# Optimization experiments

Measured on AMD Instinct MI355X. Metric: run time of the kernel, lower is better.

The kernel has to match this reference:

```python
import jax, jax.numpy as jnp
import numpy as np

B, OBS, ACT, NT, E = 4096, 512, 64, 10, 16
DREP, DH, DK = 1024, 1024, 512  # rep dim, expert hidden, key/value dim


def setup_inputs() -> dict:
    key = jax.random.key(0)
    ks = jax.random.split(key, 24)
    s = 0.02
    state_core = jax.random.normal(ks[0], (B, OBS), jnp.float32)
    task_ids = jax.random.randint(ks[1], (B,), 0, NT)
    onehot = jax.nn.one_hot(task_ids, NT, dtype=jnp.float32)
    state = jnp.concatenate([state_core, onehot], axis=-1)  # [B, OBS+NT]
    act = jax.random.normal(ks[2], (B, ACT), jnp.float32)
    return {
        "state": state,
        "act": act,
        "rep_W0": s * jax.random.normal(ks[3], (OBS + ACT, DREP), jnp.float32),
        "rep_b0": jnp.zeros((DREP,), jnp.float32),
        "rep_W1": s * jax.random.normal(ks[4], (DREP, DREP), jnp.float32),
        "rep_b1": jnp.zeros((DREP,), jnp.float32),
        "emb": 0.5 * jnp.ones((NT, DK), jnp.float32),
        "Wk0": s * jax.random.normal(ks[5], (E, DREP, DH), jnp.float32),
        "bk0": jnp.zeros((E, DH), jnp.float32),
        "Wk1": s * jax.random.normal(ks[6], (E, DH, DK), jnp.float32),
        "bk1": jnp.zeros((E, DK), jnp.float32),
        "Wv0": s * jax.random.normal(ks[7], (E, DREP, DH), jnp.float32),
        "bv0": jnp.zeros((E, DH), jnp.float32),
        "Wv1": s * jax.random.normal(ks[8], (E, DH, DK), jnp.float32),
        "bv1": jnp.zeros((E, DK), jnp.float32),
        "Wt0": s * jax.random.normal(ks[9], (DK, 512), jnp.float32),
        "bt0": jnp.zeros((512,), jnp.float32),
        "Wt1": s * jax.random.normal(ks[10], (512, 256), jnp.float32),
        "bt1": jnp.zeros((256,), jnp.float32),
        "Wt2": s * jax.random.normal(ks[11], (256, 1), jnp.float32),
        "bt2": jnp.zeros((1,), jnp.float32),
    }


def reference(state, act, rep_W0, rep_b0, rep_W1, rep_b1, emb,
              Wk0, bk0, Wk1, bk1, Wv0, bv0, Wv1, bv1,
              Wt0, bt0, Wt1, bt1, Wt2, bt2):
    num_tasks = emb.shape[0]
    task = jnp.argmax(state[:, -num_tasks:], axis=-1)  # one-hot -> index (== torch.nonzero)
    s = state[:, :-num_tasks]
    # representation: mlp([obs+act, 1024, 1024]) -> relu then identity
    x = jnp.concatenate([s, act], axis=-1)
    rep = jax.nn.relu(x @ rep_W0 + rep_b0) @ rep_W1 + rep_b1  # [B, DREP]
    query = jnp.tanh(emb[task])  # [B, DK]
    # all experts batched (original loops in Python over E tiny MLPs)
    hk = jax.nn.relu(jnp.einsum('bd,edh->ebh', rep, Wk0) + bk0[:, None, :])
    keys = jnp.einsum('ebh,ehk->ebk', hk, Wk1) + bk1[:, None, :]   # [E,B,DK]
    hv = jax.nn.relu(jnp.einsum('bd,edh->ebh', rep, Wv0) + bv0[:, None, :])
    vals = jnp.einsum('ebh,ehk->ebk', hv, Wv1) + bv1[:, None, :]   # [E,B,DK]
    logits = jnp.einsum('bk,ebk->be', query, keys)                 # [B,E]
    attn = jax.nn.softmax(logits, axis=1)
    tower_in = jnp.einsum('be,ebk->bk', attn, vals)                # [B,DK]
    h = jax.nn.relu(tower_in @ Wt0 + bt0)
    h = jax.nn.relu(h @ Wt1 + bt1)
    q = jnp.squeeze(h @ Wt2 + bt2, -1)                             # [B]
    expert_loss = -jnp.mean(
        jnp.sum(jnp.clip(jnp.log(attn + 1e-10), -6.0, 0.0), axis=-1) * 0.3)
    return q, expert_loss
```

## Files before the change

kernel.cpp:

```cpp
#include <hip/hip_runtime.h>
#include <cstdint>
#include <cstddef>

#define NB   4096
#define OBS  512
#define NACT 64
#define NT   10
#define NE   16
#define DREP 1024
#define DH   1024
#define DK   512
#define SLD  (OBS + NT)
#define XK   (OBS + NACT)

typedef short s8v __attribute__((ext_vector_type(8)));
typedef float f4v __attribute__((ext_vector_type(4)));

__device__ __forceinline__ unsigned short f2bf(float f) {
  union { float f; unsigned int u; } v; v.f = f;
  unsigned int u = v.u;
  unsigned int r = (u + 0x7FFFu + ((u >> 16) & 1u)) >> 16;
  return (unsigned short)r;
}
__device__ __forceinline__ float bf2f(unsigned short h) {
  union { unsigned int u; float f; } v; v.u = ((unsigned int)h) << 16;
  return v.f;
}

__device__ __forceinline__ void gload_lds16(const unsigned short* gp, const unsigned short* lp) {
  __builtin_amdgcn_global_load_lds(
      (const __attribute__((address_space(1))) void*)(uintptr_t)gp,
      (__attribute__((address_space(3))) void*)(unsigned int)(uintptr_t)lp,
      16, 0, 0);
}

template <int BM, int BN, int MODE, int RELU, int LDA, int LDB, int KK>
__global__ void __launch_bounds__(256)
gemm_k(const unsigned short* __restrict__ A,
       const unsigned short* __restrict__ Bt,
       const float* __restrict__ bias,
       unsigned short* __restrict__ outB, int ldo,
       const float* __restrict__ qk1, const int* __restrict__ task,
       float* __restrict__ logits, int eBase,
       const float* __restrict__ attn, float* __restrict__ cio)
{
  constexpr int FM = BM / 32;
  constexpr int FN = BN / 32;
  constexpr int CA = BM / 64;
  constexpr int CB = BN / 64;

  __shared__ __align__(16) unsigned short As[BM * 32];
  __shared__ __align__(16) unsigned short Bs[BN * 32];

  const int tid  = threadIdx.x;
  const int wave = tid >> 6;
  const int lane = tid & 63;
  const int wm = wave >> 1, wn = wave & 1;

  const int rowBase = blockIdx.x * BM;
  const int colBase = blockIdx.y * BN;

  int eg = 0;
  if (MODE == 1) {
    eg = blockIdx.z;
    Bt  += (size_t)eg * (DREP * DH);
    bias += eg * DH;
    qk1 += (size_t)eg * (NT * DH);
  }
  if (MODE == 2) {
    eg = eBase + blockIdx.z;
    Bt  += (size_t)eg * (DREP * DH);
    bias += eg * DH;
    outB += (size_t)blockIdx.z * DH;
  }
  if (MODE == 3) {
    int kz = blockIdx.z;
    A  += (size_t)kz * KK;
    Bt += (size_t)kz * KK;
  }

  f4v acc[FM][FN];
#pragma unroll
  for (int m = 0; m < FM; ++m)
#pragma unroll
    for (int n = 0; n < FN; ++n) acc[m][n] = f4v{0.f, 0.f, 0.f, 0.f};

  const int sRow = lane >> 2;
  const int sSw  = ((lane & 3) ^ ((sRow >> 1) & 3)) * 8;
  const unsigned short* Ag = A  + (size_t)rowBase * LDA + sSw;
  const unsigned short* Bg = Bt + (size_t)colBase * LDB + sSw;

  const int fr   = lane & 15;
  const int koSw = (((lane >> 4) ^ ((fr >> 1) & 3)) * 8);

  for (int kt = 0; kt < KK; kt += 32) {
    __syncthreads();
#pragma unroll
    for (int j = 0; j < CA; ++j) {
      int chunk = wave * CA + j;
      gload_lds16(Ag + (size_t)(chunk * 16 + sRow) * LDA + kt, As + chunk * 512);
    }
#pragma unroll
    for (int j = 0; j < CB; ++j) {
      int chunk = wave * CB + j;
      gload_lds16(Bg + (size_t)(chunk * 16 + sRow) * LDB + kt, Bs + chunk * 512);
    }
    __syncthreads();

    s8v av[FM], bv[FN];
#pragma unroll
    for (int m = 0; m < FM; ++m)
      av[m] = *reinterpret_cast<const s8v*>(&As[(wm * (BM / 2) + m * 16 + fr) * 32 + koSw]);
#pragma unroll
    for (int n = 0; n < FN; ++n)
      bv[n] = *reinterpret_cast<const s8v*>(&Bs[(wn * (BN / 2) + n * 16 + fr) * 32 + koSw]);
#pragma unroll
    for (int m = 0; m < FM; ++m)
#pragma unroll
      for (int n = 0; n < FN; ++n)
        acc[m][n] = __builtin_amdgcn_mfma_f32_16x16x32_bf16(av[m], bv[n], acc[m][n], 0, 0, 0);
  }

  const int cr = (lane >> 4) * 4;
  const int cc = lane & 15;

  int gcn[FN];
  float bcol[FN];
#pragma unroll
  for (int n = 0; n < FN; ++n) {
    gcn[n] = colBase + wn * (BN / 2) + n * 16 + cc;
    bcol[n] = (MODE == 3) ? 0.f : bias[gcn[n]];
  }

  if (MODE == 0 || MODE == 2) {
#pragma unroll
    for (int m = 0; m < FM; ++m)
#pragma unroll
      for (int r = 0; r < 4; ++r) {
        int gr = rowBase + wm * (BM / 2) + m * 16 + cr + r;
        float aw = 1.f;
        if (MODE == 2) aw = attn[gr * NE + eg];
#pragma unroll
        for (int n = 0; n < FN; ++n) {
          float v = acc[m][n][r] + bcol[n];
          if (RELU) v = fmaxf(v, 0.f);
          if (MODE == 2) v *= aw;
          outB[(size_t)gr * ldo + gcn[n]] = f2bf(v);
        }
      }
  }

  if (MODE == 1) {
#pragma unroll
    for (int m = 0; m < FM; ++m)
#pragma unroll
      for (int r = 0; r < 4; ++r) {
        int gr = rowBase + wm * (BM / 2) + m * 16 + cr + r;
        int t = task[gr];
        const float* qrow = qk1 + (size_t)t * DH;
        float s = 0.f;
#pragma unroll
        for (int n = 0; n < FN; ++n) {
          float v = fmaxf(acc[m][n][r] + bcol[n], 0.f);
          s += v * qrow[gcn[n]];
        }
#pragma unroll
        for (int off = 1; off < 16; off <<= 1) s += __shfl_xor(s, off, 64);
        if (cc == 0) atomicAdd(&logits[gr * NE + eg], s);
      }
  }

  if (MODE == 3) {
#pragma unroll
    for (int m = 0; m < FM; ++m)
#pragma unroll
      for (int r = 0; r < 4; ++r) {
        int gr = rowBase + wm * (BM / 2) + m * 16 + cr + r;
#pragma unroll
        for (int n = 0; n < FN; ++n)
          atomicAdd(&cio[(size_t)gr * DK + gcn[n]], acc[m][n][r]);
      }
  }
}

__global__ void task_k(const float* __restrict__ state, int* __restrict__ task) {
  int b = blockIdx.x * blockDim.x + threadIdx.x;
  if (b >= NB) return;
  const float* p = state + (size_t)b * SLD + OBS;
  float best = p[0]; int bi = 0;
  for (int j = 1; j < NT; ++j) { float v = p[j]; if (v > best) { best = v; bi = j; } }
  task[b] = bi;
}

__global__ void buildx_k(const float* __restrict__ state, const float* __restrict__ act,
                         unsigned short* __restrict__ x) {
  int idx = blockIdx.x * blockDim.x + threadIdx.x;
  if (idx >= NB * XK) return;
  int b = idx / XK, j = idx - b * XK;
  float v = (j < OBS) ? state[(size_t)b * SLD + j] : act[(size_t)b * NACT + (j - OBS)];
  x[idx] = f2bf(v);
}

__global__ void prep_emb_k(const float* __restrict__ emb, const float* __restrict__ bk1,
                           float* __restrict__ Qt, float* __restrict__ qb) {
  int t = blockIdx.x;
  __shared__ float qsh[DK];
  for (int k = threadIdx.x; k < DK; k += 256) {
    float v = tanhf(emb[t * DK + k]);
    Qt[t * DK + k] = v;
    qsh[k] = v;
  }
  __syncthreads();
  int wave = threadIdx.x >> 6, lane = threadIdx.x & 63;
  for (int e = wave; e < NE; e += 4) {
    float s = 0.f;
    for (int k = lane; k < DK; k += 64) s += qsh[k] * bk1[e * DK + k];
    for (int off = 1; off < 64; off <<= 1) s += __shfl_xor(s, off, 64);
    if (lane == 0) qb[e * NT + t] = s;
  }
}

__global__ void qk1_k(const float* __restrict__ Wk1, const float* __restrict__ Qt,
                      float* __restrict__ qk1) {
  int w = (blockIdx.x * blockDim.x + threadIdx.x) >> 6;
  int lane = threadIdx.x & 63;
  if (w >= NE * DH) return;
  int e = w >> 10, h = w & (DH - 1);
  const float* wrow = Wk1 + ((size_t)e * DH + h) * DK + lane * 8;
  float wv[8];
#pragma unroll
  for (int j = 0; j < 8; ++j) wv[j] = wrow[j];
#pragma unroll
  for (int t = 0; t < NT; ++t) {
    const float* qrow = Qt + t * DK + lane * 8;
    float s = 0.f;
#pragma unroll
    for (int j = 0; j < 8; ++j) s += wv[j] * qrow[j];
#pragma unroll
    for (int off = 1; off < 64; off <<= 1) s += __shfl_xor(s, off, 64);
    if (lane == 0) qk1[((size_t)e * NT + t) * DH + h] = s;
  }
}

__global__ void __launch_bounds__(256)
convT_k(const float* __restrict__ src, unsigned short* __restrict__ dst,
        int N, long sBS, long dBS, int dLd) {
  __shared__ float tile[64][65];
  int e = blockIdx.z;
  int n0 = blockIdx.x * 64, k0 = blockIdx.y * 64;
  src += (size_t)e * sBS + (size_t)k0 * N + n0;
  dst += (size_t)e * dBS + (size_t)n0 * dLd + k0;
  int t = threadIdx.x;
  int c4 = t & 15, kr = t >> 4;
#pragma unroll
  for (int i = 0; i < 4; ++i) {
    float4 v = *(const float4*)(src + (size_t)(kr + i * 16) * N + c4 * 4);
    tile[kr + i * 16][c4 * 4 + 0] = v.x;
    tile[kr + i * 16][c4 * 4 + 1] = v.y;
    tile[kr + i * 16][c4 * 4 + 2] = v.z;
    tile[kr + i * 16][c4 * 4 + 3] = v.w;
  }
  __syncthreads();
  int sub = t & 7, nl = t >> 3;
#pragma unroll
  for (int pass = 0; pass < 2; ++pass) {
    int n = nl + pass * 32;
    unsigned short v8[8];
#pragma unroll
    for (int j = 0; j < 8; ++j) v8[j] = f2bf(tile[sub * 8 + j][n]);
    *reinterpret_cast<s8v*>(dst + (size_t)n * dLd + sub * 8) =
        *reinterpret_cast<const s8v*>(v8);
  }
}

__global__ void softmax_k(const float* __restrict__ logits, const float* __restrict__ qb,
                          const int* __restrict__ task, float* __restrict__ attn,
                          float* __restrict__ lossOut) {
  int b = blockIdx.x * blockDim.x + threadIdx.x;
  int t = task[b];
  float l[NE];
  float mx = -1e30f;
#pragma unroll
  for (int e = 0; e < NE; ++e) { l[e] = logits[b * NE + e] + qb[e * NT + t]; mx = fmaxf(mx, l[e]); }
  float s = 0.f;
#pragma unroll
  for (int e = 0; e < NE; ++e) { l[e] = expf(l[e] - mx); s += l[e]; }
  float inv = 1.f / s;
  float loss = 0.f;
#pragma unroll
  for (int e = 0; e < NE; ++e) {
    float a = l[e] * inv;
    attn[b * NE + e] = a;
    float lg = logf(a + 1e-10f);
    loss += fminf(fmaxf(lg, -6.f), 0.f);
  }
  for (int off = 1; off < 64; off <<= 1) loss += __shfl_xor(loss, off, 64);
  if ((threadIdx.x & 63) == 0) atomicAdd(lossOut, loss * (-0.3f / NB));
}

__global__ void towerbias_k(const float* __restrict__ attn, const float* __restrict__ bv1,
                            float* __restrict__ towerin) {
  int idx = blockIdx.x * blockDim.x + threadIdx.x;
  if (idx >= NB * DK) return;
  int b = idx >> 9, k = idx & (DK - 1);
  float s = 0.f;
#pragma unroll
  for (int e = 0; e < NE; ++e) s += attn[b * NE + e] * bv1[e * DK + k];
  towerin[idx] = s;
}

__global__ void cvt_ti_k(const float* __restrict__ twin, unsigned short* __restrict__ ti) {
  int idx = (blockIdx.x * blockDim.x + threadIdx.x) * 8;
  if (idx >= NB * DK) return;
  float4 a = *(const float4*)(twin + idx);
  float4 b = *(const float4*)(twin + idx + 4);
  unsigned short v8[8] = {f2bf(a.x), f2bf(a.y), f2bf(a.z), f2bf(a.w),
                          f2bf(b.x), f2bf(b.y), f2bf(b.z), f2bf(b.w)};
  *reinterpret_cast<s8v*>(ti + idx) = *reinterpret_cast<const s8v*>(v8);
}

__global__ void qfinal_k(const unsigned short* __restrict__ h2, const float* __restrict__ Wt2,
                         const float* __restrict__ bt2, float* __restrict__ out) {
  int w = (blockIdx.x * blockDim.x + threadIdx.x) >> 6;
  int lane = threadIdx.x & 63;
  if (w >= NB) return;
  float s = 0.f;
#pragma unroll
  for (int j = 0; j < 4; ++j) {
    int k = lane * 4 + j;
    s += bf2f(h2[(size_t)w * 256 + k]) * Wt2[k];
  }
  for (int off = 1; off < 64; off <<= 1) s += __shfl_xor(s, off, 64);
  if (lane == 0) out[w] = s + bt2[0];
}

extern "C" void kernel_launch(void* const* d_in, const int* in_sizes, int n_in,
                              void* d_out, int out_size, void* d_ws, size_t ws_size,
                              hipStream_t stream) {
  const float* state  = (const float*)d_in[0];
  const float* act    = (const float*)d_in[1];
  const float* rep_W0 = (const float*)d_in[2];
  const float* rep_b0 = (const float*)d_in[3];
  const float* rep_W1 = (const float*)d_in[4];
  const float* rep_b1 = (const float*)d_in[5];
  const float* emb    = (const float*)d_in[6];
  const float* Wk0    = (const float*)d_in[7];
  const float* bk0    = (const float*)d_in[8];
  const float* Wk1    = (const float*)d_in[9];
  const float* bk1    = (const float*)d_in[10];
  const float* Wv0    = (const float*)d_in[11];
  const float* bv0    = (const float*)d_in[12];
  const float* Wv1    = (const float*)d_in[13];
  const float* bv1    = (const float*)d_in[14];
  const float* Wt0    = (const float*)d_in[15];
  const float* bt0    = (const float*)d_in[16];
  const float* Wt1    = (const float*)d_in[17];
  const float* bt1    = (const float*)d_in[18];
  const float* Wt2    = (const float*)d_in[19];
  const float* bt2    = (const float*)d_in[20];
  float* out = (float*)d_out;

  char* wsb = (char*)d_ws;
  size_t off = 0;
  auto alloc = [&](size_t bytes) -> void* {
    void* p = wsb + off;
    off += (bytes + 255) & ~(size_t)255;
    return p;
  };
  unsigned short* Ap    = (unsigned short*)alloc((size_t)NB * 8192 * 2);
  unsigned short* Wk0t  = (unsigned short*)alloc((size_t)NE * DREP * DH * 2);
  unsigned short* Wv0t  = (unsigned short*)alloc((size_t)NE * DREP * DH * 2);
  unsigned short* Wv1t  = (unsigned short*)alloc((size_t)DK * (NE * DH) * 2);
  unsigned short* h0    = (unsigned short*)alloc((size_t)NB * DREP * 2);
  unsigned short* rep   = (unsigned short*)alloc((size_t)NB * DREP * 2);
  float*          twin  = (float*)alloc((size_t)NB * DK * 4);
  unsigned short* xbuf  = (unsigned short*)alloc((size_t)NB * XK * 2);
  unsigned short* ti    = (unsigned short*)alloc((size_t)NB * DK * 2);
  unsigned short* h1    = (unsigned short*)alloc((size_t)NB * 512 * 2);
  unsigned short* h2    = (unsigned short*)alloc((size_t)NB * 256 * 2);
  unsigned short* rW1t  = (unsigned short*)alloc((size_t)DREP * DREP * 2);
  unsigned short* rW0t  = (unsigned short*)alloc((size_t)DREP * XK * 2);
  float*          qk1   = (float*)alloc((size_t)NE * NT * DH * 4);
  unsigned short* Wt0t  = (unsigned short*)alloc((size_t)512 * 512 * 2);
  unsigned short* Wt1t  = (unsigned short*)alloc((size_t)256 * 512 * 2);
  float*          logits= (float*)alloc((size_t)NB * NE * 4);
  float*          attn  = (float*)alloc((size_t)NB * NE * 4);
  float*          Qt    = (float*)alloc((size_t)NT * DK * 4);
  int*            task  = (int*)alloc((size_t)NB * 4);
  float*          qb    = (float*)alloc((size_t)NE * NT * 4);

  hipMemsetAsync(logits, 0, (size_t)NB * NE * 4, stream);
  hipMemsetAsync(out + NB, 0, sizeof(float), stream);

  task_k<<<NB / 256, 256, 0, stream>>>(state, task);
  buildx_k<<<(NB * XK + 255) / 256, 256, 0, stream>>>(state, act, xbuf);
  prep_emb_k<<<NT, 256, 0, stream>>>(emb, bk1, Qt, qb);
  qk1_k<<<NE * DH / 4, 256, 0, stream>>>(Wk1, Qt, qk1);

  convT_k<<<dim3(DREP / 64, XK / 64, 1), 256, 0, stream>>>(rep_W0, rW0t, DREP, 0, 0, XK);
  convT_k<<<dim3(DREP / 64, DREP / 64, 1), 256, 0, stream>>>(rep_W1, rW1t, DREP, 0, 0, DREP);
  convT_k<<<dim3(DH / 64, DREP / 64, NE), 256, 0, stream>>>(Wk0, Wk0t, DH, (long)DREP * DH, (long)DREP * DH, DREP);
  convT_k<<<dim3(DH / 64, DREP / 64, NE), 256, 0, stream>>>(Wv0, Wv0t, DH, (long)DREP * DH, (long)DREP * DH, DREP);
  convT_k<<<dim3(DK / 64, DH / 64, NE), 256, 0, stream>>>(Wv1, Wv1t, DK, (long)DH * DK, 1024L, NE * DH);
  convT_k<<<dim3(512 / 64, 512 / 64, 1), 256, 0, stream>>>(Wt0, Wt0t, 512, 0, 0, 512);
  convT_k<<<dim3(256 / 64, 512 / 64, 1), 256, 0, stream>>>(Wt1, Wt1t, 256, 0, 0, 512);

  gemm_k<128, 128, 0, 1, XK, XK, XK><<<dim3(NB / 128, DREP / 128, 1), 256, 0, stream>>>(
      xbuf, rW0t, rep_b0, h0, DREP, nullptr, nullptr, nullptr, 0, nullptr, nullptr);
  gemm_k<128, 128, 0, 0, DREP, DREP, DREP><<<dim3(NB / 128, DREP / 128, 1), 256, 0, stream>>>(
      h0, rW1t, rep_b1, rep, DREP, nullptr, nullptr, nullptr, 0, nullptr, nullptr);

  gemm_k<128, 128, 1, 1, DREP, DREP, DREP><<<dim3(NB / 128, DH / 128, NE), 256, 0, stream>>>(
      rep, Wk0t, bk0, nullptr, 0, qk1, task, logits, 0, nullptr, nullptr);

  softmax_k<<<NB / 256, 256, 0, stream>>>(logits, qb, task, attn, out + NB);
  towerbias_k<<<NB * DK / 256, 256, 0, stream>>>(attn, bv1, twin);

  for (int g = 0; g < 2; ++g) {
    gemm_k<128, 128, 2, 1, DREP, DREP, DREP><<<dim3(NB / 128, DH / 128, 8), 256, 0, stream>>>(
        rep, Wv0t, bv0, Ap, 8192, nullptr, nullptr, nullptr, g * 8, attn, nullptr);
    gemm_k<128, 128, 3, 0, 8192, NE * DH, 2048><<<dim3(NB / 128, DK / 128, 4), 256, 0, stream>>>(
        Ap, Wv1t + (size_t)g * 8192, nullptr, nullptr, 0,
        nullptr, nullptr, nullptr, 0, nullptr, twin);
  }
  cvt_ti_k<<<(NB * DK / 8 + 255) / 256, 256, 0, stream>>>(twin, ti);

  gemm_k<64, 64, 0, 1, DK, DK, DK><<<dim3(NB / 64, 512 / 64, 1), 256, 0, stream>>>(
      ti, Wt0t, bt0, h1, 512, nullptr, nullptr, nullptr, 0, nullptr, nullptr);
  gemm_k<64, 64, 0, 1, 512, 512, 512><<<dim3(NB / 64, 256 / 64, 1), 256, 0, stream>>>(
      h1, Wt1t, bt1, h2, 256, nullptr, nullptr, nullptr, 0, nullptr, nullptr);
  qfinal_k<<<NB / 4, 256, 0, stream>>>(h2, Wt2, bt2, out);
}
```

Baseline: 877.0 us.

## Double-buffer GEMM LDS tiles and replace split-K atomics with partial buffers

The shared GEMM kernel now uses two LDS buffers and prefetches the next K tile while computing the current one, so there is one barrier per iteration instead of two. The split-K value-projection GEMM no longer issues fp32 atomicAdds. Each K split writes to its own partial buffer: the second group accumulates with a plain read-modify-write, and the conversion kernel sums the four partials plus the bias term. This removes atomic contention at the cost of 32 MB of extra workspace and more memory traffic in the final reduction. LDS use per block doubles, which may lower occupancy.

```diff
diff --git a/kernel.cpp b/kernel.cpp
--- a/kernel.cpp
+++ b/kernel.cpp
@@ -48,9 +48,10 @@
   constexpr int FN = BN / 32;
   constexpr int CA = BM / 64;
   constexpr int CB = BN / 64;
-
-  __shared__ __align__(16) unsigned short As[BM * 32];
-  __shared__ __align__(16) unsigned short Bs[BN * 32];
+  constexpr int NTILES = KK / 32;
+
+  __shared__ __align__(16) unsigned short As[2][BM * 32];
+  __shared__ __align__(16) unsigned short Bs[2][BN * 32];
 
   const int tid  = threadIdx.x;
   const int wave = tid >> 6;
@@ -73,10 +74,10 @@
     bias += eg * DH;
     outB += (size_t)blockIdx.z * DH;
   }
-  if (MODE == 3) {
-    int kz = blockIdx.z;
-    A  += (size_t)kz * KK;
-    Bt += (size_t)kz * KK;
+  if (MODE == 3 || MODE == 4) {
+    A   += (size_t)blockIdx.z * KK;
+    Bt  += (size_t)blockIdx.z * KK;
+    cio += (size_t)blockIdx.z * NB * DK;
   }
 
   f4v acc[FM][FN];
@@ -93,27 +94,43 @@
   const int fr   = lane & 15;
   const int koSw = (((lane >> 4) ^ ((fr >> 1) & 3)) * 8);
 
-  for (int kt = 0; kt < KK; kt += 32) {
-    __syncthreads();
-#pragma unroll
-    for (int j = 0; j < CA; ++j) {
-      int chunk = wave * CA + j;
-      gload_lds16(Ag + (size_t)(chunk * 16 + sRow) * LDA + kt, As + chunk * 512);
+#pragma unroll
+  for (int j = 0; j < CA; ++j) {
+    int chunk = wave * CA + j;
+    gload_lds16(Ag + (size_t)(chunk * 16 + sRow) * LDA, As[0] + chunk * 512);
+  }
+#pragma unroll
+  for (int j = 0; j < CB; ++j) {
+    int chunk = wave * CB + j;
+    gload_lds16(Bg + (size_t)(chunk * 16 + sRow) * LDB, Bs[0] + chunk * 512);
+  }
+
+  for (int t = 0; t < NTILES; ++t) {
+    const int buf = t & 1;
+    __builtin_amdgcn_s_waitcnt(0);
+    __builtin_amdgcn_s_barrier();
+
+    if (t + 1 < NTILES) {
+      const int kt = (t + 1) * 32;
+#pragma unroll
+      for (int j = 0; j < CA; ++j) {
+        int chunk = wave * CA + j;
+        gload_lds16(Ag + (size_t)(chunk * 16 + sRow) * LDA + kt, As[buf ^ 1] + chunk * 512);
+      }
+#pragma unroll
+      for (int j = 0; j < CB; ++j) {
+        int chunk = wave * CB + j;
+        gload_lds16(Bg + (size_t)(chunk * 16 + sRow) * LDB + kt, Bs[buf ^ 1] + chunk * 512);
+      }
     }
-#pragma unroll
-    for (int j = 0; j < CB; ++j) {
-      int chunk = wave * CB + j;
-      gload_lds16(Bg + (size_t)(chunk * 16 + sRow) * LDB + kt, Bs + chunk * 512);
-    }
-    __syncthreads();
 
     s8v av[FM], bv[FN];
 #pragma unroll
     for (int m = 0; m < FM; ++m)
-      av[m] = *reinterpret_cast<const s8v*>(&As[(wm * (BM / 2) + m * 16 + fr) * 32 + koSw]);
+      av[m] = *reinterpret_cast<const s8v*>(&As[buf][(wm * (BM / 2) + m * 16 + fr) * 32 + koSw]);
 #pragma unroll
     for (int n = 0; n < FN; ++n)
-      bv[n] = *reinterpret_cast<const s8v*>(&Bs[(wn * (BN / 2) + n * 16 + fr) * 32 + koSw]);
+      bv[n] = *reinterpret_cast<const s8v*>(&Bs[buf][(wn * (BN / 2) + n * 16 + fr) * 32 + koSw]);
 #pragma unroll
     for (int m = 0; m < FM; ++m)
 #pragma unroll
@@ -129,7 +146,7 @@
 #pragma unroll
   for (int n = 0; n < FN; ++n) {
     gcn[n] = colBase + wn * (BN / 2) + n * 16 + cc;
-    bcol[n] = (MODE == 3) ? 0.f : bias[gcn[n]];
+    bcol[n] = (MODE >= 3) ? 0.f : bias[gcn[n]];
   }
 
   if (MODE == 0 || MODE == 2) {
@@ -170,15 +187,18 @@
       }
   }
 
-  if (MODE == 3) {
+  if (MODE == 3 || MODE == 4) {
 #pragma unroll
     for (int m = 0; m < FM; ++m)
 #pragma unroll
       for (int r = 0; r < 4; ++r) {
         int gr = rowBase + wm * (BM / 2) + m * 16 + cr + r;
 #pragma unroll
-        for (int n = 0; n < FN; ++n)
-          atomicAdd(&cio[(size_t)gr * DK + gcn[n]], acc[m][n][r]);
+        for (int n = 0; n < FN; ++n) {
+          float v = acc[m][n][r];
+          if (MODE == 4) v += cio[(size_t)gr * DK + gcn[n]];
+          cio[(size_t)gr * DK + gcn[n]] = v;
+        }
       }
   }
 }
@@ -309,13 +329,22 @@
   towerin[idx] = s;
 }
 
-__global__ void cvt_ti_k(const float* __restrict__ twin, unsigned short* __restrict__ ti) {
+__global__ void cvt_ti_k(const float* __restrict__ twin, const float* __restrict__ P,
+                         unsigned short* __restrict__ ti) {
   int idx = (blockIdx.x * blockDim.x + threadIdx.x) * 8;
   if (idx >= NB * DK) return;
-  float4 a = *(const float4*)(twin + idx);
-  float4 b = *(const float4*)(twin + idx + 4);
-  unsigned short v8[8] = {f2bf(a.x), f2bf(a.y), f2bf(a.z), f2bf(a.w),
-                          f2bf(b.x), f2bf(b.y), f2bf(b.z), f2bf(b.w)};
+  float v[8];
+#pragma unroll
+  for (int j = 0; j < 8; ++j) v[j] = twin[idx + j];
+#pragma unroll
+  for (int c = 0; c < 4; ++c) {
+    const float* p = P + (size_t)c * NB * DK + idx;
+#pragma unroll
+    for (int j = 0; j < 8; ++j) v[j] += p[j];
+  }
+  unsigned short v8[8];
+#pragma unroll
+  for (int j = 0; j < 8; ++j) v8[j] = f2bf(v[j]);
   *reinterpret_cast<s8v*>(ti + idx) = *reinterpret_cast<const s8v*>(v8);
 }
 
@@ -371,6 +400,7 @@
   unsigned short* Wk0t  = (unsigned short*)alloc((size_t)NE * DREP * DH * 2);
   unsigned short* Wv0t  = (unsigned short*)alloc((size_t)NE * DREP * DH * 2);
   unsigned short* Wv1t  = (unsigned short*)alloc((size_t)DK * (NE * DH) * 2);
+  float*          P     = (float*)alloc((size_t)4 * NB * DK * 4);
   unsigned short* h0    = (unsigned short*)alloc((size_t)NB * DREP * 2);
   unsigned short* rep   = (unsigned short*)alloc((size_t)NB * DREP * 2);
   float*          twin  = (float*)alloc((size_t)NB * DK * 4);
@@ -419,11 +449,14 @@
   for (int g = 0; g < 2; ++g) {
     gemm_k<128, 128, 2, 1, DREP, DREP, DREP><<<dim3(NB / 128, DH / 128, 8), 256, 0, stream>>>(
         rep, Wv0t, bv0, Ap, 8192, nullptr, nullptr, nullptr, g * 8, attn, nullptr);
-    gemm_k<128, 128, 3, 0, 8192, NE * DH, 2048><<<dim3(NB / 128, DK / 128, 4), 256, 0, stream>>>(
-        Ap, Wv1t + (size_t)g * 8192, nullptr, nullptr, 0,
-        nullptr, nullptr, nullptr, 0, nullptr, twin);
-  }
-  cvt_ti_k<<<(NB * DK / 8 + 255) / 256, 256, 0, stream>>>(twin, ti);
+    if (g == 0)
+      gemm_k<128, 128, 3, 0, 8192, NE * DH, 2048><<<dim3(NB / 128, DK / 128, 4), 256, 0, stream>>>(
+          Ap, Wv1t, nullptr, nullptr, 0, nullptr, nullptr, nullptr, 0, nullptr, P);
+    else
+      gemm_k<128, 128, 4, 0, 8192, NE * DH, 2048><<<dim3(NB / 128, DK / 128, 4), 256, 0, stream>>>(
+          Ap, Wv1t + (size_t)8192, nullptr, nullptr, 0, nullptr, nullptr, nullptr, 0, nullptr, P);
+  }
+  cvt_ti_k<<<(NB * DK / 8 + 255) / 256, 256, 0, stream>>>(twin, P, ti);
 
   gemm_k<64, 64, 0, 1, DK, DK, DK><<<dim3(NB / 64, 512 / 64, 1), 256, 0, stream>>>(
       ti, Wt0t, bt0, h1, 512, nullptr, nullptr, nullptr, 0, nullptr, nullptr);
```

After: 841.7 us. -4.0%, faster.
